# Performance work log

Hardware: AMD Instinct MI355X
Metric: run time of the kernel (lower is better)

The kernel has to match this reference:

```python
import jax, jax.numpy as jnp
import numpy as np

D = 1024       # embedding_dim
H = 16         # num_attention_heads
B = 2
S = 2048       # seq_len == context_len


def setup_inputs() -> dict:
    key = jax.random.key(0)
    k1, k2, k3 = jax.random.split(key, 3)
    X = jax.random.normal(k1, (B, S, D), dtype=jnp.float32)
    W_qkv = jax.random.normal(k2, (D, 3 * D), dtype=jnp.float32) * 0.02
    b_qkv = jnp.zeros((3 * D,), dtype=jnp.float32)
    W_out = jax.random.normal(k3, (D, D), dtype=jnp.float32) * 0.02
    b_out = jnp.zeros((D,), dtype=jnp.float32)
    return {"X": X, "W_qkv": W_qkv, "b_qkv": b_qkv, "W_out": W_out, "b_out": b_out}


def reference(X, W_qkv, b_qkv, W_out, b_out):
    b, s, d = X.shape
    hd = d // H
    # fused QKV projection (GPT-2 Conv1D == x @ W + b)
    qkv = X @ W_qkv + b_qkv                       # [b, s, 3d]
    q, k, v = jnp.split(qkv, 3, axis=2)
    # [b, h, s, hd]
    q = q.reshape(b, s, H, hd).transpose(0, 2, 1, 3)
    k = k.reshape(b, s, H, hd).transpose(0, 2, 1, 3)
    v = v.reshape(b, s, H, hd).transpose(0, 2, 1, 3)
    # NOTE: source scales by rsqrt(embedding_dim), not head_dim
    scale = 1.0 / jnp.sqrt(jnp.float32(d))
    scores = jnp.einsum("bhqd,bhkd->bhqk", q, k) * scale
    causal = jnp.tril(jnp.ones((s, s), dtype=bool))
    scores = jnp.where(causal[None, None], scores, -jnp.inf)
    # attention_dropout applied pre-softmax in source; identity at eval (p used here = 0)
    probs = jax.nn.softmax(scores, axis=-1)
    attn = jnp.einsum("bhqk,bhkd->bhqd", probs, v)
    attn = attn.transpose(0, 2, 1, 3).reshape(b, s, d)
    out = attn @ W_out + b_out                    # outwards proj; dropout eval = identity
    return out
```

## Files before the change

### kernel.cpp

```cpp
#include <hip/hip_runtime.h>

#define S_LEN 2048
#define DIM   1024
#define NHEAD 16
#define HDIM  64

typedef __attribute__((ext_vector_type(8))) short  short8;
typedef __attribute__((ext_vector_type(4))) float  floatx4;
typedef __attribute__((ext_vector_type(4))) unsigned short ushort4v;

#define Q_PRESCALE 0.045084220027780106f

__device__ inline unsigned short f2bf(float f) {
  unsigned v = __builtin_bit_cast(unsigned, f);
  v += 0x7FFFu + ((v >> 16) & 1u);
  return (unsigned short)(v >> 16);
}

__global__ __launch_bounds__(256) void cvtT_kernel(
    const float* __restrict__ in, unsigned short* __restrict__ out, int K, int N) {
  __shared__ unsigned short tile[32][33];
  int n0 = blockIdx.x * 32, k0 = blockIdx.y * 32;
  int tx = threadIdx.x, ty = threadIdx.y;
#pragma unroll
  for (int i = 0; i < 32; i += 8)
    tile[ty + i][tx] = f2bf(in[(size_t)(k0 + ty + i) * N + n0 + tx]);
  __syncthreads();
#pragma unroll
  for (int i = 0; i < 32; i += 8)
    out[(size_t)(n0 + ty + i) * K + k0 + tx] = tile[tx][ty + i];
}

__global__ __launch_bounds__(256) void gemm_qkv_kernel(
    const float* __restrict__ X,
    const unsigned short* __restrict__ Wt,
    const float* __restrict__ bias,
    unsigned short* __restrict__ Qg,
    unsigned short* __restrict__ Kg,
    unsigned short* __restrict__ Vgt,
    int g0, int G) {
  __shared__ __align__(16) unsigned short As[64][72];
  __shared__ __align__(16) unsigned short Bs[64][72];
  const int tn = blockIdx.x;
  const int section = tn / G, within = tn % G;
  const int n0 = section * 1024 + (g0 + within) * 64;
  const int m0 = blockIdx.y * 64;
  const int t = threadIdx.x, lane = t & 63, wave = t >> 6;
  const int quad = lane >> 4, l16 = lane & 15;

  floatx4 acc[4];
#pragma unroll
  for (int i = 0; i < 4; i++) acc[i] = (floatx4){0.f, 0.f, 0.f, 0.f};

  for (int k0 = 0; k0 < DIM; k0 += 64) {
#pragma unroll
    for (int i = 0; i < 2; i++) {
      int v = t + i * 256;
      int row = v >> 3, cc = (v & 7) * 8;
      float4 f0 = *(const float4*)&X[(size_t)(m0 + row) * DIM + k0 + cc];
      float4 f1 = *(const float4*)&X[(size_t)(m0 + row) * DIM + k0 + cc + 4];
      short8 o;
      o[0] = (short)f2bf(f0.x); o[1] = (short)f2bf(f0.y);
      o[2] = (short)f2bf(f0.z); o[3] = (short)f2bf(f0.w);
      o[4] = (short)f2bf(f1.x); o[5] = (short)f2bf(f1.y);
      o[6] = (short)f2bf(f1.z); o[7] = (short)f2bf(f1.w);
      *(short8*)&As[row][cc] = o;
      *(short8*)&Bs[row][cc] = *(const short8*)&Wt[(size_t)(n0 + row) * DIM + k0 + cc];
    }
    __syncthreads();
    short8 a0 = *(const short8*)&As[wave * 16 + l16][quad * 8];
    short8 a1 = *(const short8*)&As[wave * 16 + l16][32 + quad * 8];
#pragma unroll
    for (int nt = 0; nt < 4; nt++) {
      short8 b0 = *(const short8*)&Bs[nt * 16 + l16][quad * 8];
      short8 b1 = *(const short8*)&Bs[nt * 16 + l16][32 + quad * 8];
      acc[nt] = __builtin_amdgcn_mfma_f32_16x16x32_bf16(a0, b0, acc[nt], 0, 0, 0);
      acc[nt] = __builtin_amdgcn_mfma_f32_16x16x32_bf16(a1, b1, acc[nt], 0, 0, 0);
    }
    __syncthreads();
  }

  const int mbase = m0 + wave * 16 + quad * 4;
  const int b = mbase >> 11, sbase = mbase & 2047;
  const int y = b * G + within;
  if (section == 2) {
#pragma unroll
    for (int nt = 0; nt < 4; nt++) {
      int hdi = nt * 16 + l16;
      float bv = bias[n0 + hdi];
      ushort4v o;
#pragma unroll
      for (int r = 0; r < 4; r++) o[r] = f2bf(acc[nt][r] + bv);
      *(ushort4v*)&Vgt[((size_t)y * HDIM + hdi) * S_LEN + sbase] = o;
    }
  } else if (section == 0) {
#pragma unroll
    for (int nt = 0; nt < 4; nt++) {
      int hdi = nt * 16 + l16;
      float bv = bias[n0 + hdi];
#pragma unroll
      for (int r = 0; r < 4; r++)
        Qg[((size_t)y * S_LEN + sbase + r) * HDIM + hdi] =
            f2bf((acc[nt][r] + bv) * Q_PRESCALE);
    }
  } else {
#pragma unroll
    for (int nt = 0; nt < 4; nt++) {
      int hdi = nt * 16 + l16;
      float bv = bias[n0 + hdi];
#pragma unroll
      for (int r = 0; r < 4; r++)
        Kg[((size_t)y * S_LEN + sbase + r) * HDIM + hdi] = f2bf(acc[nt][r] + bv);
    }
  }
}

__global__ __launch_bounds__(256) void attn_kernel(
    const unsigned short* __restrict__ Qg,
    const unsigned short* __restrict__ Kg,
    const unsigned short* __restrict__ Vgt,
    unsigned short* __restrict__ attnB,
    int g0, int G) {
  __shared__ __align__(16) unsigned short Ks[64][72];
  __shared__ __align__(16) unsigned short Vt[80][72];
  __shared__ __align__(16) unsigned short Ps[4][16][72];

  const int y = blockIdx.y;
  const int b = y / G, hl = y % G;
  const int pairIdx = blockIdx.x;
  const int t = threadIdx.x;
  const int lane = t & 63, wave = t >> 6;
  const int quad = lane >> 4, l16 = lane & 15;

  const unsigned short* Qh = Qg + (size_t)y * S_LEN * HDIM;
  const unsigned short* Kh = Kg + (size_t)y * S_LEN * HDIM;
  const unsigned short* Vh = Vgt + (size_t)y * HDIM * S_LEN;

  {
    int rr = t >> 4, cb = (t & 15) * 4;
    ushort4v ov;
    unsigned short vv = (rr == 0) ? (unsigned short)0x3F80 : (unsigned short)0;
    ov[0] = vv; ov[1] = vv; ov[2] = vv; ov[3] = vv;
    *(ushort4v*)&Vt[64 + rr][cb] = ov;
  }

#pragma unroll
  for (int pass = 0; pass < 2; pass++) {
    const int qt = (pass == 0) ? pairIdx : (31 - pairIdx);
    const int q0 = qt * 64;

    short8 aq0 = *(const short8*)&Qh[(size_t)(q0 + wave * 16 + l16) * HDIM + quad * 8];
    short8 aq1 = *(const short8*)&Qh[(size_t)(q0 + wave * 16 + l16) * HDIM + 32 + quad * 8];

    floatx4 o_acc[5];
#pragma unroll
    for (int dt = 0; dt < 5; dt++) o_acc[dt] = (floatx4){0.f, 0.f, 0.f, 0.f};

    for (int j0 = 0; j0 <= q0; j0 += 64) {
#pragma unroll
      for (int i = 0; i < 2; i++) {
        int v = t + i * 256;
        int row = v >> 3, cc = (v & 7) * 8;
        *(short8*)&Ks[row][cc] = *(const short8*)&Kh[(size_t)(j0 + row) * HDIM + cc];
        *(short8*)&Vt[row][cc] = *(const short8*)&Vh[(size_t)row * S_LEN + j0 + cc];
      }
      __syncthreads();

      floatx4 sc[4];
#pragma unroll
      for (int nt = 0; nt < 4; nt++) {
        sc[nt] = (floatx4){0.f, 0.f, 0.f, 0.f};
        short8 b0 = *(const short8*)&Ks[nt * 16 + l16][quad * 8];
        short8 b1 = *(const short8*)&Ks[nt * 16 + l16][32 + quad * 8];
        sc[nt] = __builtin_amdgcn_mfma_f32_16x16x32_bf16(aq0, b0, sc[nt], 0, 0, 0);
        sc[nt] = __builtin_amdgcn_mfma_f32_16x16x32_bf16(aq1, b1, sc[nt], 0, 0, 0);
      }

      if (j0 == q0) {
#pragma unroll
        for (int nt = 0; nt < 4; nt++) {
          int keyl = nt * 16 + l16;
#pragma unroll
          for (int r = 0; r < 4; r++) {
            int ql = wave * 16 + quad * 4 + r;
            float p = exp2f(sc[nt][r]);
            p = (keyl <= ql) ? p : 0.f;
            Ps[wave][quad * 4 + r][nt * 16 + l16] = f2bf(p);
          }
        }
      } else {
#pragma unroll
        for (int nt = 0; nt < 4; nt++) {
#pragma unroll
          for (int r = 0; r < 4; r++)
            Ps[wave][quad * 4 + r][nt * 16 + l16] = f2bf(exp2f(sc[nt][r]));
        }
      }
      short8 ap0 = *(const short8*)&Ps[wave][l16][quad * 8];
      short8 ap1 = *(const short8*)&Ps[wave][l16][32 + quad * 8];

#pragma unroll
      for (int dt = 0; dt < 5; dt++) {
        short8 bv0 = *(const short8*)&Vt[dt * 16 + l16][quad * 8];
        short8 bv1 = *(const short8*)&Vt[dt * 16 + l16][32 + quad * 8];
        o_acc[dt] = __builtin_amdgcn_mfma_f32_16x16x32_bf16(ap0, bv0, o_acc[dt], 0, 0, 0);
        o_acc[dt] = __builtin_amdgcn_mfma_f32_16x16x32_bf16(ap1, bv1, o_acc[dt], 0, 0, 0);
      }
      __syncthreads();
    }

    float linv[4];
#pragma unroll
    for (int r = 0; r < 4; r++)
      linv[r] = 1.0f / __shfl(o_acc[4][r], quad << 4);

#pragma unroll
    for (int dt = 0; dt < 4; dt++) {
#pragma unroll
      for (int r = 0; r < 4; r++) {
        int qg = q0 + wave * 16 + quad * 4 + r;
        attnB[(size_t)(b * S_LEN + qg) * DIM + (g0 + hl) * HDIM + dt * 16 + l16] =
            f2bf(o_acc[dt][r] * linv[r]);
      }
    }
  }
}

__global__ __launch_bounds__(256) void gemm_out_kernel(
    const unsigned short* __restrict__ A,
    const unsigned short* __restrict__ Wt,
    const float* __restrict__ bias,
    float* __restrict__ outp) {
  __shared__ __align__(16) unsigned short As[64][72];
  __shared__ __align__(16) unsigned short Bs[64][72];
  const int m0 = blockIdx.y * 64, n0 = blockIdx.x * 64;
  const int t = threadIdx.x, lane = t & 63, wave = t >> 6;
  const int quad = lane >> 4, l16 = lane & 15;

  floatx4 acc[4];
#pragma unroll
  for (int i = 0; i < 4; i++) acc[i] = (floatx4){0.f, 0.f, 0.f, 0.f};

  for (int k0 = 0; k0 < DIM; k0 += 64) {
#pragma unroll
    for (int i = 0; i < 2; i++) {
      int v = t + i * 256;
      int row = v >> 3, cc = (v & 7) * 8;
      *(short8*)&As[row][cc] = *(const short8*)&A[(size_t)(m0 + row) * DIM + k0 + cc];
      *(short8*)&Bs[row][cc] = *(const short8*)&Wt[(size_t)(n0 + row) * DIM + k0 + cc];
    }
    __syncthreads();
    short8 a0 = *(const short8*)&As[wave * 16 + l16][quad * 8];
    short8 a1 = *(const short8*)&As[wave * 16 + l16][32 + quad * 8];
#pragma unroll
    for (int nt = 0; nt < 4; nt++) {
      short8 b0 = *(const short8*)&Bs[nt * 16 + l16][quad * 8];
      short8 b1 = *(const short8*)&Bs[nt * 16 + l16][32 + quad * 8];
      acc[nt] = __builtin_amdgcn_mfma_f32_16x16x32_bf16(a0, b0, acc[nt], 0, 0, 0);
      acc[nt] = __builtin_amdgcn_mfma_f32_16x16x32_bf16(a1, b1, acc[nt], 0, 0, 0);
    }
    __syncthreads();
  }

#pragma unroll
  for (int nt = 0; nt < 4; nt++) {
    int n = n0 + nt * 16 + l16;
    float bv = bias[n];
#pragma unroll
    for (int r = 0; r < 4; r++) {
      int m = m0 + wave * 16 + quad * 4 + r;
      outp[(size_t)m * DIM + n] = acc[nt][r] + bv;
    }
  }
}

extern "C" void kernel_launch(void* const* d_in, const int* in_sizes, int n_in,
                              void* d_out, int out_size, void* d_ws, size_t ws_size,
                              hipStream_t stream) {
  const float* X    = (const float*)d_in[0];
  const float* Wqkv = (const float*)d_in[1];
  const float* bqkv = (const float*)d_in[2];
  const float* Wout = (const float*)d_in[3];
  const float* bout = (const float*)d_in[4];
  float* outp = (float*)d_out;

  unsigned short* Wqkvt = (unsigned short*)d_ws;
  unsigned short* Woutt = Wqkvt + (size_t)3145728;
  unsigned short* attnB = Woutt + (size_t)1048576;
  unsigned short* Qbase = attnB + (size_t)4194304;

  const size_t baseB   = (size_t)(3145728 + 1048576 + 4194304) * 2;
  const size_t perHead = (size_t)3 * 2 * S_LEN * HDIM * 2;
  int G = 1;
  if      (ws_size >= baseB + 16 * perHead) G = 16;
  else if (ws_size >= baseB + 8 * perHead)  G = 8;
  else if (ws_size >= baseB + 4 * perHead)  G = 4;
  else if (ws_size >= baseB + 2 * perHead)  G = 2;

  unsigned short* Qg  = Qbase;
  unsigned short* Kg  = Qg + (size_t)2 * G * S_LEN * HDIM;
  unsigned short* Vgt = Kg + (size_t)2 * G * S_LEN * HDIM;

  cvtT_kernel<<<dim3(3072 / 32, 1024 / 32), dim3(32, 8), 0, stream>>>(Wqkv, Wqkvt, 1024, 3072);
  cvtT_kernel<<<dim3(1024 / 32, 1024 / 32), dim3(32, 8), 0, stream>>>(Wout, Woutt, 1024, 1024);

  for (int g0 = 0; g0 < NHEAD; g0 += G) {
    gemm_qkv_kernel<<<dim3(3 * G, 4096 / 64), 256, 0, stream>>>(
        X, Wqkvt, bqkv, Qg, Kg, Vgt, g0, G);
    attn_kernel<<<dim3(16, 2 * G), 256, 0, stream>>>(
        Qg, Kg, Vgt, attnB, g0, G);
  }
  gemm_out_kernel<<<dim3(1024 / 64, 4096 / 64), 256, 0, stream>>>(attnB, Woutt, bout, outp);
}
```

Before: 210.3 us.

## Use 128x128 async-LDS GEMM tiles with pre-converted bf16 X and single-pass heads

```diff
diff --git a/kernel.cpp b/kernel.cpp
--- a/kernel.cpp
+++ b/kernel.cpp
@@ -15,6 +15,26 @@
   unsigned v = __builtin_bit_cast(unsigned, f);
   v += 0x7FFFu + ((v >> 16) & 1u);
   return (unsigned short)(v >> 16);
+}
+
+__device__ inline void async16(const unsigned short* g, unsigned short* l) {
+  __builtin_amdgcn_global_load_lds(
+      (const __attribute__((address_space(1))) unsigned int*)g,
+      (__attribute__((address_space(3))) unsigned int*)l, 16, 0, 0);
+}
+
+__global__ __launch_bounds__(256) void cvt_kernel(
+    const float* __restrict__ in, unsigned short* __restrict__ out, int n) {
+  int i = (blockIdx.x * 256 + threadIdx.x) * 8;
+  if (i >= n) return;
+  float4 a = *(const float4*)&in[i];
+  float4 b = *(const float4*)&in[i + 4];
+  short8 o;
+  o[0] = (short)f2bf(a.x); o[1] = (short)f2bf(a.y);
+  o[2] = (short)f2bf(a.z); o[3] = (short)f2bf(a.w);
+  o[4] = (short)f2bf(b.x); o[5] = (short)f2bf(b.y);
+  o[6] = (short)f2bf(b.z); o[7] = (short)f2bf(b.w);
+  *(short8*)&out[i] = o;
 }
 
 __global__ __launch_bounds__(256) void cvtT_kernel(
@@ -29,6 +49,112 @@
 #pragma unroll
   for (int i = 0; i < 32; i += 8)
     out[(size_t)(n0 + ty + i) * K + k0 + tx] = tile[tx][ty + i];
+}
+
+#define GEMM128_BODY(APTR, BPTR)                                                   \
+  __shared__ __align__(16) unsigned short As[128][64];                             \
+  __shared__ __align__(16) unsigned short Bs[128][64];                             \
+  const int m0 = blockIdx.y * 128, n0 = blockIdx.x * 128;                          \
+  const int t = threadIdx.x, lane = t & 63, wave = t >> 6;                         \
+  const int quad = lane >> 4, l16 = lane & 15;                                     \
+  const int wm = (wave >> 1) * 64, wn = (wave & 1) * 64;                           \
+  const int lr = lane >> 3, lc = lane & 7, sc8 = (lc ^ lr) * 8;                    \
+  const int sw = l16 & 7;                                                          \
+  const int pA0 = (quad ^ sw) * 8, pA1 = ((4 + quad) ^ sw) * 8;                    \
+  floatx4 acc[4][4];                                                               \
+  _Pragma("unroll") for (int mi = 0; mi < 4; mi++)                                 \
+      _Pragma("unroll") for (int ni = 0; ni < 4; ni++)                             \
+          acc[mi][ni] = (floatx4){0.f, 0.f, 0.f, 0.f};                             \
+  for (int k0 = 0; k0 < DIM; k0 += 64) {                                           \
+    _Pragma("unroll") for (int i = 0; i < 4; i++) {                                \
+      int rb = wave * 32 + i * 8;                                                  \
+      async16(&APTR[(size_t)(m0 + rb + lr) * DIM + k0 + sc8], &As[rb][0]);         \
+      async16(&BPTR[(size_t)(n0 + rb + lr) * DIM + k0 + sc8], &Bs[rb][0]);         \
+    }                                                                              \
+    __syncthreads();                                                               \
+    short8 a0[4], a1[4];                                                           \
+    _Pragma("unroll") for (int mi = 0; mi < 4; mi++) {                             \
+      int row = wm + mi * 16 + l16;                                                \
+      a0[mi] = *(const short8*)&As[row][pA0];                                      \
+      a1[mi] = *(const short8*)&As[row][pA1];                                      \
+    }                                                                              \
+    _Pragma("unroll") for (int ni = 0; ni < 4; ni++) {                             \
+      int row = wn + ni * 16 + l16;                                                \
+      short8 b0 = *(const short8*)&Bs[row][pA0];                                   \
+      short8 b1 = *(const short8*)&Bs[row][pA1];                                   \
+      _Pragma("unroll") for (int mi = 0; mi < 4; mi++) {                           \
+        acc[mi][ni] = __builtin_amdgcn_mfma_f32_16x16x32_bf16(a0[mi], b0, acc[mi][ni], 0, 0, 0); \
+        acc[mi][ni] = __builtin_amdgcn_mfma_f32_16x16x32_bf16(a1[mi], b1, acc[mi][ni], 0, 0, 0); \
+      }                                                                            \
+    }                                                                              \
+    __syncthreads();                                                               \
+  }
+
+__global__ __launch_bounds__(256) void gemm_qkv128(
+    const unsigned short* __restrict__ Xb,
+    const unsigned short* __restrict__ Wt,
+    const float* __restrict__ bias,
+    unsigned short* __restrict__ Qg,
+    unsigned short* __restrict__ Kg,
+    unsigned short* __restrict__ Vgt) {
+  GEMM128_BODY(Xb, Wt)
+  const int section = n0 >> 10;
+  const int head = ((n0 + wn) >> 6) & 15;
+#pragma unroll
+  for (int mi = 0; mi < 4; mi++) {
+    int mg = m0 + wm + mi * 16 + quad * 4;
+    int bb = mg >> 11, sb = mg & 2047;
+    size_t y = (size_t)bb * NHEAD + head;
+    if (section == 2) {
+#pragma unroll
+      for (int ni = 0; ni < 4; ni++) {
+        int hdi = ni * 16 + l16;
+        float bv = bias[n0 + wn + hdi];
+        ushort4v o;
+#pragma unroll
+        for (int r = 0; r < 4; r++) o[r] = f2bf(acc[mi][ni][r] + bv);
+        *(ushort4v*)&Vgt[(y * HDIM + hdi) * S_LEN + sb] = o;
+      }
+    } else if (section == 0) {
+#pragma unroll
+      for (int ni = 0; ni < 4; ni++) {
+        int hdi = ni * 16 + l16;
+        float bv = bias[n0 + wn + hdi];
+#pragma unroll
+        for (int r = 0; r < 4; r++)
+          Qg[(y * S_LEN + sb + r) * HDIM + hdi] = f2bf((acc[mi][ni][r] + bv) * Q_PRESCALE);
+      }
+    } else {
+#pragma unroll
+      for (int ni = 0; ni < 4; ni++) {
+        int hdi = ni * 16 + l16;
+        float bv = bias[n0 + wn + hdi];
+#pragma unroll
+        for (int r = 0; r < 4; r++)
+          Kg[(y * S_LEN + sb + r) * HDIM + hdi] = f2bf(acc[mi][ni][r] + bv);
+      }
+    }
+  }
+}
+
+__global__ __launch_bounds__(256) void gemm_out128(
+    const unsigned short* __restrict__ A,
+    const unsigned short* __restrict__ Wt,
+    const float* __restrict__ bias,
+    float* __restrict__ outp) {
+  GEMM128_BODY(A, Wt)
+#pragma unroll
+  for (int ni = 0; ni < 4; ni++) {
+    int n = n0 + wn + ni * 16 + l16;
+    float bv = bias[n];
+#pragma unroll
+    for (int mi = 0; mi < 4; mi++) {
+      int mg = m0 + wm + mi * 16 + quad * 4;
+#pragma unroll
+      for (int r = 0; r < 4; r++)
+        outp[(size_t)(mg + r) * DIM + n] = acc[mi][ni][r] + bv;
+    }
+  }
 }
 
 __global__ __launch_bounds__(256) void gemm_qkv_kernel(
@@ -226,54 +352,6 @@
   }
 }
 
-__global__ __launch_bounds__(256) void gemm_out_kernel(
-    const unsigned short* __restrict__ A,
-    const unsigned short* __restrict__ Wt,
-    const float* __restrict__ bias,
-    float* __restrict__ outp) {
-  __shared__ __align__(16) unsigned short As[64][72];
-  __shared__ __align__(16) unsigned short Bs[64][72];
-  const int m0 = blockIdx.y * 64, n0 = blockIdx.x * 64;
-  const int t = threadIdx.x, lane = t & 63, wave = t >> 6;
-  const int quad = lane >> 4, l16 = lane & 15;
-
-  floatx4 acc[4];
-#pragma unroll
-  for (int i = 0; i < 4; i++) acc[i] = (floatx4){0.f, 0.f, 0.f, 0.f};
-
-  for (int k0 = 0; k0 < DIM; k0 += 64) {
-#pragma unroll
-    for (int i = 0; i < 2; i++) {
-      int v = t + i * 256;
-      int row = v >> 3, cc = (v & 7) * 8;
-      *(short8*)&As[row][cc] = *(const short8*)&A[(size_t)(m0 + row) * DIM + k0 + cc];
-      *(short8*)&Bs[row][cc] = *(const short8*)&Wt[(size_t)(n0 + row) * DIM + k0 + cc];
-    }
-    __syncthreads();
-    short8 a0 = *(const short8*)&As[wave * 16 + l16][quad * 8];
-    short8 a1 = *(const short8*)&As[wave * 16 + l16][32 + quad * 8];
-#pragma unroll
-    for (int nt = 0; nt < 4; nt++) {
-      short8 b0 = *(const short8*)&Bs[nt * 16 + l16][quad * 8];
-      short8 b1 = *(const short8*)&Bs[nt * 16 + l16][32 + quad * 8];
-      acc[nt] = __builtin_amdgcn_mfma_f32_16x16x32_bf16(a0, b0, acc[nt], 0, 0, 0);
-      acc[nt] = __builtin_amdgcn_mfma_f32_16x16x32_bf16(a1, b1, acc[nt], 0, 0, 0);
-    }
-    __syncthreads();
-  }
-
-#pragma unroll
-  for (int nt = 0; nt < 4; nt++) {
-    int n = n0 + nt * 16 + l16;
-    float bv = bias[n];
-#pragma unroll
-    for (int r = 0; r < 4; r++) {
-      int m = m0 + wave * 16 + quad * 4 + r;
-      outp[(size_t)m * DIM + n] = acc[nt][r] + bv;
-    }
-  }
-}
-
 extern "C" void kernel_launch(void* const* d_in, const int* in_sizes, int n_in,
                               void* d_out, int out_size, void* d_ws, size_t ws_size,
                               hipStream_t stream) {
@@ -287,28 +365,24 @@
   unsigned short* Wqkvt = (unsigned short*)d_ws;
   unsigned short* Woutt = Wqkvt + (size_t)3145728;
   unsigned short* attnB = Woutt + (size_t)1048576;
-  unsigned short* Qbase = attnB + (size_t)4194304;
-
-  const size_t baseB   = (size_t)(3145728 + 1048576 + 4194304) * 2;
-  const size_t perHead = (size_t)3 * 2 * S_LEN * HDIM * 2;
-  int G = 1;
-  if      (ws_size >= baseB + 16 * perHead) G = 16;
-  else if (ws_size >= baseB + 8 * perHead)  G = 8;
-  else if (ws_size >= baseB + 4 * perHead)  G = 4;
-  else if (ws_size >= baseB + 2 * perHead)  G = 2;
-
-  unsigned short* Qg  = Qbase;
-  unsigned short* Kg  = Qg + (size_t)2 * G * S_LEN * HDIM;
-  unsigned short* Vgt = Kg + (size_t)2 * G * S_LEN * HDIM;
+  unsigned short* Qg    = attnB + (size_t)4194304;
+  unsigned short* Kg    = Qg + (size_t)4194304;
+  unsigned short* Vgt   = Kg + (size_t)4194304;
+  unsigned short* Xb    = Vgt + (size_t)4194304;
+
+  const bool bigWs = ws_size >= (size_t)48 * 1024 * 1024;
 
   cvtT_kernel<<<dim3(3072 / 32, 1024 / 32), dim3(32, 8), 0, stream>>>(Wqkv, Wqkvt, 1024, 3072);
   cvtT_kernel<<<dim3(1024 / 32, 1024 / 32), dim3(32, 8), 0, stream>>>(Wout, Woutt, 1024, 1024);
 
-  for (int g0 = 0; g0 < NHEAD; g0 += G) {
-    gemm_qkv_kernel<<<dim3(3 * G, 4096 / 64), 256, 0, stream>>>(
-        X, Wqkvt, bqkv, Qg, Kg, Vgt, g0, G);
-    attn_kernel<<<dim3(16, 2 * G), 256, 0, stream>>>(
-        Qg, Kg, Vgt, attnB, g0, G);
-  }
-  gemm_out_kernel<<<dim3(1024 / 64, 4096 / 64), 256, 0, stream>>>(attnB, Woutt, bout, outp);
-}
+  if (bigWs) {
+    cvt_kernel<<<4194304 / (256 * 8), 256, 0, stream>>>(X, Xb, 4194304);
+    gemm_qkv128<<<dim3(3072 / 128, 4096 / 128), 256, 0, stream>>>(
+        Xb, Wqkvt, bqkv, Qg, Kg, Vgt);
+  } else {
+    gemm_qkv_kernel<<<dim3(48, 64), 256, 0, stream>>>(
+        X, Wqkvt, bqkv, Qg, Kg, Vgt, 0, 16);
+  }
+  attn_kernel<<<dim3(16, 32), 256, 0, stream>>>(Qg, Kg, Vgt, attnB, 0, 16);
+  gemm_out128<<<dim3(1024 / 128, 4096 / 128), 256, 0, stream>>>(attnB, Woutt, bout, outp);
+}
```

Measured after the change: 206.7 us. Within noise of the previous version (-1.7%).
